# Optimization experiments

Measured on AMD Instinct MI355X. Metric: run time of the kernel, lower is better.

## Reference

```python
import jax, jax.numpy as jnp
import numpy as np

T = 16384      # total packed tokens
C = 1024       # d_model
H = 16         # n_head
HD = C // H    # head dim = 64
N_SEG = 32     # number of equal varlen segments
SEG = T // N_SEG


def setup_inputs() -> dict:
    key = jax.random.key(0)
    k1, k2, k3 = jax.random.split(key, 3)
    x = jax.random.normal(k1, (T, C), dtype=jnp.float32)
    w_attn = jax.random.normal(k2, (C, 3 * C), dtype=jnp.float32) * (1.0 / np.sqrt(C))
    w_proj = jax.random.normal(k3, (C, C), dtype=jnp.float32) * (1.0 / np.sqrt(C))
    # boundary indices for torch.tensor_split -> 32 equal segments of SEG tokens
    split_sections = (jnp.arange(1, N_SEG) * SEG).astype(jnp.int64)
    return {"x": x, "w_attn": w_attn, "w_proj": w_proj, "split_sections": split_sections}


def reference(x, w_attn, w_proj, split_sections):
    # x: [T, C] packed tokens; split_sections: 31 boundaries -> 32 equal segments
    n_seg = int(np.asarray(split_sections).shape[0]) + 1
    seg = x.shape[0] // n_seg
    qkv = x @ w_attn                                   # [T, 3C]
    q, k, v = jnp.split(qkv, 3, axis=-1)               # each [T, C]

    def heads(t):
        # [T, C] -> [H, n_seg, seg, HD]  (block-diagonal segment layout)
        return t.reshape(x.shape[0], H, HD).transpose(1, 0, 2).reshape(H, n_seg, seg, HD)

    q, k, v = heads(q), heads(k), heads(v)
    scale = 1.0 / np.sqrt(HD)
    att = jnp.einsum('hnqd,hnkd->hnqk', q, k) * scale  # [H, n_seg, seg, seg]
    att = jax.nn.softmax(att, axis=-1)
    y = jnp.einsum('hnqk,hnkd->hnqd', att, v)          # [H, n_seg, seg, HD]
    y = y.reshape(H, x.shape[0], HD).transpose(1, 0, 2).reshape(x.shape[0], C)
    return y @ w_proj                                  # [T, C]
```

## Files before the change

kernel.cpp:

```cpp
#include <hip/hip_runtime.h>
#include <hip/hip_bf16.h>
#include <stdint.h>

typedef __attribute__((ext_vector_type(8))) short short8;
typedef __attribute__((ext_vector_type(4))) short short4_t;
typedef __attribute__((ext_vector_type(4))) float float4_t;

#define GLOAD_LDS16(gp, lp)                                                              \
  __builtin_amdgcn_global_load_lds((const __attribute__((address_space(1))) unsigned int*)(gp), \
                                   (__attribute__((address_space(3))) unsigned int*)(lp), \
                                   16, 0, 0)

__device__ __forceinline__ float4_t mfma_bf16(short8 a, short8 b, float4_t c) {
  return __builtin_amdgcn_mfma_f32_16x16x32_bf16(a, b, c, 0, 0, 0);
}

__device__ __forceinline__ short f2bf(float f) {
  union { float f; unsigned int u; } v; v.f = f;
  unsigned int r = v.u + 0x7fff + ((v.u >> 16) & 1);
  return (short)(r >> 16);
}

__device__ __forceinline__ float red_sum16(float v) {
  v += __shfl_xor(v, 1);
  v += __shfl_xor(v, 2);
  v += __shfl_xor(v, 4);
  v += __shfl_xor(v, 8);
  return v;
}

__device__ __forceinline__ long swz_col(long colbase64, int chunk, int sub, int row) {
  return colbase64 + ((chunk ^ (row & 7)) << 3) + sub;
}

__global__ __launch_bounds__(256) void conv_swz(const float* __restrict__ in,
                                                short* __restrict__ out, long nchunks) {
  for (long ch = (long)blockIdx.x * blockDim.x + threadIdx.x; ch < nchunks;
       ch += (long)gridDim.x * blockDim.x) {
    long r  = ch >> 7;
    int cir = (int)(ch & 127);
    int pc  = (cir & ~3) | ((cir & 3) ^ (((int)r >> 1) & 3));
    const float* src = in + ch * 8;
    short8 o;
#pragma unroll
    for (int j = 0; j < 8; ++j) o[j] = f2bf(src[j]);
    *(short8*)&out[r * 1024 + pc * 8] = o;
  }
}

__global__ __launch_bounds__(256) void transpose_conv(const float* __restrict__ in,
                                                      short* __restrict__ out,
                                                      int R, int C) {
  __shared__ short tile[32][33];
  int c0 = blockIdx.x * 32;
  int r0 = blockIdx.y * 32;
  int tx = threadIdx.x;
  int ty = threadIdx.y;
#pragma unroll
  for (int i = 0; i < 4; ++i)
    tile[ty + i * 8][tx] = f2bf(in[(long)(r0 + ty + i * 8) * C + c0 + tx]);
  __syncthreads();
#pragma unroll
  for (int i = 0; i < 4; ++i) {
    int n   = c0 + ty + i * 8;
    long cc = (long)r0 + ((((tx >> 3) ^ ((n >> 1) & 3))) << 3) + (tx & 7);
    out[(long)n * R + cc] = tile[tx][ty + i * 8];
  }
}

template <int MODE>
__global__ __launch_bounds__(512, 2) void gemm256(const short* __restrict__ A, long lda,
                                                  const short* __restrict__ Bt, long ldb,
                                                  void* __restrict__ Cv,
                                                  short* __restrict__ vT,
                                                  int M, int N, int K) {
  __shared__ __align__(16) short As[4][256 * 32];
  __shared__ __align__(16) short Bs[4][256 * 32];

  const int tid  = threadIdx.x;
  const int wave = tid >> 6;
  const int lane = tid & 63;
  const int rA   = lane & 15;
  const int q4   = lane >> 4;
  const int wm   = (wave >> 2) * 128;
  const int wn   = (wave & 3) * 64;

  const int nbx = N >> 8;
  const int nwg = nbx * (M >> 8);
  const int bid = (int)blockIdx.y * nbx + (int)blockIdx.x;
  const int cpx = nwg >> 3;
  const int swz = (bid & 7) * cpx + (bid >> 3);
  const long m0 = (long)(swz / nbx) * 256;
  const long n0 = (long)(swz % nbx) * 256;

  const short* Ag = A  + (m0 + (tid >> 2)) * lda + (tid & 3) * 8;
  const short* Bg = Bt + (n0 + (tid >> 2)) * ldb + (tid & 3) * 8;

#define STAGE_A(u)                                                          \
  {                                                                         \
    const int slot_ = (u) & 3;                                              \
    GLOAD_LDS16(Ag + (u) * 32,             &As[slot_][wave * 512]);         \
    GLOAD_LDS16(Ag + 128 * lda + (u) * 32, &As[slot_][4096 + wave * 512]);  \
  }
#define STAGE_B(u)                                                          \
  {                                                                         \
    const int slot_ = (u) & 3;                                              \
    GLOAD_LDS16(Bg + (u) * 32,             &Bs[slot_][wave * 512]);         \
    GLOAD_LDS16(Bg + 128 * ldb + (u) * 32, &Bs[slot_][4096 + wave * 512]);  \
  }

  float4_t acc[8][4];
#pragma unroll
  for (int i = 0; i < 8; ++i)
#pragma unroll
    for (int j = 0; j < 4; ++j) acc[i][j] = (float4_t){0.f, 0.f, 0.f, 0.f};

  const int nt = K >> 5;

  STAGE_A(0); STAGE_B(0);
  STAGE_A(1); STAGE_B(1);
  STAGE_A(2); STAGE_B(2);
  asm volatile("s_waitcnt vmcnt(8)" ::: "memory");
  __builtin_amdgcn_s_barrier();

  const int cswz = q4 ^ ((rA >> 1) & 3);

  for (int u = 0; u < nt; ++u) {
    const int slot = u & 3;
    short8 af[4], bfr[4];
#pragma unroll
    for (int mi = 0; mi < 4; ++mi)
      af[mi] = *(const short8*)&As[slot][((wm + mi * 16 + rA) * 4 + cswz) * 8];
#pragma unroll
    for (int ni = 0; ni < 4; ++ni)
      bfr[ni] = *(const short8*)&Bs[slot][((wn + ni * 16 + rA) * 4 + cswz) * 8];
    if (u + 3 < nt) STAGE_A(u + 3);
    __builtin_amdgcn_s_barrier();
    __builtin_amdgcn_s_setprio(1);
#pragma unroll
    for (int mi = 0; mi < 4; ++mi)
#pragma unroll
      for (int ni = 0; ni < 4; ++ni)
        acc[mi][ni] = mfma_bf16(af[mi], bfr[ni], acc[mi][ni]);
    __builtin_amdgcn_s_setprio(0);
    __builtin_amdgcn_s_barrier();
#pragma unroll
    for (int mi = 0; mi < 4; ++mi)
      af[mi] = *(const short8*)&As[slot][((wm + 64 + mi * 16 + rA) * 4 + cswz) * 8];
    if (u + 3 < nt) STAGE_B(u + 3);
    __builtin_amdgcn_s_barrier();
    __builtin_amdgcn_s_setprio(1);
#pragma unroll
    for (int mi = 0; mi < 4; ++mi)
#pragma unroll
      for (int ni = 0; ni < 4; ++ni)
        acc[mi + 4][ni] = mfma_bf16(af[mi], bfr[ni], acc[mi + 4][ni]);
    __builtin_amdgcn_s_setprio(0);
    {
      const int rem = nt - 2 - u;
      if (rem >= 2)      asm volatile("s_waitcnt vmcnt(8)" ::: "memory");
      else if (rem == 1) asm volatile("s_waitcnt vmcnt(4)" ::: "memory");
      else               asm volatile("s_waitcnt vmcnt(0)" ::: "memory");
    }
    __builtin_amdgcn_s_barrier();
  }
#undef STAGE_A
#undef STAGE_B

  if constexpr (MODE == 1) {
    short* Cq = (short*)Cv;
    if (n0 >= 2048) {
#pragma unroll
      for (int mi = 0; mi < 8; ++mi) {
        int tbase = (int)m0 + wm + mi * 16 + q4 * 4;
        int ct    = (tbase >> 3) & 7;
#pragma unroll
        for (int ni = 0; ni < 4; ++ni) {
          int c = (int)n0 + wn + ni * 16 + rA;
          int d = c - 2048;
          long dst = (long)d * 16384 + (tbase & ~63) +
                     (((ct ^ (d & 7))) << 3) + (tbase & 7);
          short4_t o;
#pragma unroll
          for (int reg = 0; reg < 4; ++reg) o[reg] = f2bf(acc[mi][ni][reg]);
          *(short4_t*)&vT[dst] = o;
        }
      }
    } else {
#pragma unroll
      for (int mi = 0; mi < 8; ++mi)
#pragma unroll
        for (int ni = 0; ni < 4; ++ni)
#pragma unroll
          for (int reg = 0; reg < 4; ++reg) {
            long t = m0 + wm + mi * 16 + q4 * 4 + reg;
            int  c = (int)n0 + wn + ni * 16 + rA;
            long cc = swz_col((long)(c & ~63), (c >> 3) & 7, c & 7, (int)t);
            Cq[t * 3072 + cc] = f2bf(acc[mi][ni][reg]);
          }
    }
  } else {
    float* Co = (float*)Cv;
    (void)vT;
#pragma unroll
    for (int mi = 0; mi < 8; ++mi)
#pragma unroll
      for (int ni = 0; ni < 4; ++ni)
#pragma unroll
        for (int reg = 0; reg < 4; ++reg) {
          long row = m0 + wm + mi * 16 + q4 * 4 + reg;
          long col = n0 + wn + ni * 16 + rA;
          Co[row * (long)N + col] = acc[mi][ni][reg];
        }
  }
}

__global__ __launch_bounds__(256, 2) void attn_kernel(short* __restrict__ qkv,
                                                      const short* __restrict__ vT) {
  __shared__ __align__(16) short Qs[128 * 64];
  __shared__ __align__(16) short Ks[2][64 * 64];
  __shared__ __align__(16) short Vt[2][64 * 64];
  __shared__ __align__(16) short Ps[128 * 72];

  const int tid  = threadIdx.x;
  const int wave = tid >> 6;
  const int lane = tid & 63;
  const int rA   = lane & 15;
  const int q4   = lane >> 4;
  const int qt   = blockIdx.x;
  const int seg  = blockIdx.y;
  const int h    = blockIdx.z;

  const long tq0  = (long)seg * 512 + qt * 128;
  const long tk0  = (long)seg * 512;
  const long hoff = (long)h * 64;

#pragma unroll
  for (int i = 0; i < 4; ++i) {
    int slot = i * 256 + tid;
    int r    = slot >> 3;
    int c    = slot & 7;
    GLOAD_LDS16(qkv + (tq0 + r) * 3072 + hoff + c * 8, &Qs[(i * 256 + wave * 64) * 8]);
  }
#pragma unroll
  for (int i = 0; i < 2; ++i) {
    int slot = i * 256 + tid;
    int r    = slot >> 3;
    int c    = slot & 7;
    GLOAD_LDS16(qkv + (tk0 + r) * 3072 + 1024 + hoff + c * 8,
                &Ks[0][(i * 256 + wave * 64) * 8]);
    GLOAD_LDS16(vT + (hoff + r) * 16384 + tk0 + c * 8,
                &Vt[0][(i * 256 + wave * 64) * 8]);
  }

  float4_t acc_o[2][4];
  float l_st[2][4];
#pragma unroll
  for (int mi = 0; mi < 2; ++mi)
#pragma unroll
    for (int di = 0; di < 4; ++di) acc_o[mi][di] = (float4_t){0.f, 0.f, 0.f, 0.f};
#pragma unroll
  for (int mi = 0; mi < 2; ++mi)
#pragma unroll
    for (int reg = 0; reg < 4; ++reg) l_st[mi][reg] = 0.f;

  for (int kt = 0; kt < 8; ++kt) {
    const int p = kt & 1;
    __syncthreads();

    if (kt < 7) {
      const long tkn = tk0 + (kt + 1) * 64;
#pragma unroll
      for (int i = 0; i < 2; ++i) {
        int slot = i * 256 + tid;
        int r    = slot >> 3;
        int c    = slot & 7;
        GLOAD_LDS16(qkv + (tkn + r) * 3072 + 1024 + hoff + c * 8,
                    &Ks[1 - p][(i * 256 + wave * 64) * 8]);
        GLOAD_LDS16(vT + (hoff + r) * 16384 + tkn + c * 8,
                    &Vt[1 - p][(i * 256 + wave * 64) * 8]);
      }
    }

    float4_t s_acc[2][4];
#pragma unroll
    for (int mi = 0; mi < 2; ++mi)
#pragma unroll
      for (int ni = 0; ni < 4; ++ni) s_acc[mi][ni] = (float4_t){0.f, 0.f, 0.f, 0.f};
#pragma unroll
    for (int kk = 0; kk < 2; ++kk) {
      int cp = (kk * 4 + q4) ^ (rA & 7);
      short8 af[2], bfr[4];
#pragma unroll
      for (int mi = 0; mi < 2; ++mi) {
        int r  = wave * 32 + mi * 16 + rA;
        af[mi] = *(const short8*)&Qs[(r * 8 + cp) * 8];
      }
#pragma unroll
      for (int ni = 0; ni < 4; ++ni) {
        int r  = ni * 16 + rA;
        bfr[ni] = *(const short8*)&Ks[p][(r * 8 + cp) * 8];
      }
#pragma unroll
      for (int mi = 0; mi < 2; ++mi)
#pragma unroll
        for (int ni = 0; ni < 4; ++ni)
          s_acc[mi][ni] = mfma_bf16(af[mi], bfr[ni], s_acc[mi][ni]);
    }

#pragma unroll
    for (int mi = 0; mi < 2; ++mi)
#pragma unroll
      for (int reg = 0; reg < 4; ++reg) {
        float rs = 0.f;
#pragma unroll
        for (int ni = 0; ni < 4; ++ni) {
          float pv = __expf(s_acc[mi][ni][reg] * 0.125f);
          s_acc[mi][ni][reg] = pv;
          rs += pv;
        }
        l_st[mi][reg] += rs;
      }

#pragma unroll
    for (int mi = 0; mi < 2; ++mi)
#pragma unroll
      for (int ni = 0; ni < 4; ++ni)
#pragma unroll
        for (int reg = 0; reg < 4; ++reg)
          Ps[(wave * 32 + mi * 16 + q4 * 4 + reg) * 72 + ni * 16 + rA] =
              f2bf(s_acc[mi][ni][reg]);

    __syncthreads();

#pragma unroll
    for (int kk = 0; kk < 2; ++kk) {
      int cp = (kk * 4 + q4) ^ (rA & 7);
      short8 af[2], bfr[4];
#pragma unroll
      for (int mi = 0; mi < 2; ++mi)
        af[mi] = *(const short8*)&Ps[(wave * 32 + mi * 16 + rA) * 72 + (kk * 4 + q4) * 8];
#pragma unroll
      for (int di = 0; di < 4; ++di)
        bfr[di] = *(const short8*)&Vt[p][((di * 16 + rA) * 8 + cp) * 8];
#pragma unroll
      for (int mi = 0; mi < 2; ++mi)
#pragma unroll
        for (int di = 0; di < 4; ++di)
          acc_o[mi][di] = mfma_bf16(af[mi], bfr[di], acc_o[mi][di]);
    }
  }

#pragma unroll
  for (int mi = 0; mi < 2; ++mi)
#pragma unroll
    for (int reg = 0; reg < 4; ++reg) {
      float l  = red_sum16(l_st[mi][reg]);
      float rl = 1.0f / l;
      long t = tq0 + wave * 32 + mi * 16 + q4 * 4 + reg;
#pragma unroll
      for (int di = 0; di < 4; ++di) {
        int c  = di * 16 + rA;
        long cc = hoff + (c & 32) +
                  (((((c >> 3) & 3) ^ (((int)t >> 1) & 3))) << 3) + (c & 7);
        qkv[t * 3072 + cc] = f2bf(acc_o[mi][di][reg] * rl);
      }
    }
}

extern "C" void kernel_launch(void* const* d_in, const int* in_sizes, int n_in,
                              void* d_out, int out_size, void* d_ws, size_t ws_size,
                              hipStream_t stream) {
  const float* x      = (const float*)d_in[0];
  const float* w_attn = (const float*)d_in[1];
  const float* w_proj = (const float*)d_in[2];
  float* out = (float*)d_out;

  short* wT_a = (short*)d_ws;
  short* wT_p = wT_a + (size_t)3072 * 1024;
  short* qkv  = wT_p + (size_t)1024 * 1024;

  short* xb = (short*)d_out;
  short* vT = xb + (size_t)16384 * 1024;

  conv_swz<<<2048, 256, 0, stream>>>(x, xb, (long)16384 * 1024 / 8);
  transpose_conv<<<dim3(3072 / 32, 1024 / 32), dim3(32, 8), 0, stream>>>(w_attn, wT_a, 1024, 3072);
  transpose_conv<<<dim3(1024 / 32, 1024 / 32), dim3(32, 8), 0, stream>>>(w_proj, wT_p, 1024, 1024);

  gemm256<1><<<dim3(3072 / 256, 16384 / 256), 512, 0, stream>>>(xb, 1024, wT_a, 1024, qkv, vT,
                                                                16384, 3072, 1024);

  attn_kernel<<<dim3(4, 32, 16), 256, 0, stream>>>(qkv, vT);

  gemm256<2><<<dim3(1024 / 256, 16384 / 256), 512, 0, stream>>>(qkv, 3072, wT_p, 1024, out, nullptr,
                                                                16384, 1024, 1024);
}
```

Before: 366.1 us.

## Software-pipeline LDS fragment loads across K-tiles in GEMM main loop

```diff
diff --git a/kernel.cpp b/kernel.cpp
--- a/kernel.cpp
+++ b/kernel.cpp
@@ -116,6 +116,7 @@
     for (int j = 0; j < 4; ++j) acc[i][j] = (float4_t){0.f, 0.f, 0.f, 0.f};
 
   const int nt = K >> 5;
+  const int cswz = q4 ^ ((rA >> 1) & 3);
 
   STAGE_A(0); STAGE_B(0);
   STAGE_A(1); STAGE_B(1);
@@ -123,46 +124,57 @@
   asm volatile("s_waitcnt vmcnt(8)" ::: "memory");
   __builtin_amdgcn_s_barrier();
 
-  const int cswz = q4 ^ ((rA >> 1) & 3);
-
-  for (int u = 0; u < nt; ++u) {
+  short8 afl[4], afh[4], bf0[4], bf1[4];
+#pragma unroll
+  for (int mi = 0; mi < 4; ++mi)
+    afl[mi] = *(const short8*)&As[0][((wm + mi * 16 + rA) * 4 + cswz) * 8];
+#pragma unroll
+  for (int ni = 0; ni < 4; ++ni)
+    bf0[ni] = *(const short8*)&Bs[0][((wn + ni * 16 + rA) * 4 + cswz) * 8];
+
+  auto tile_step = [&](int u, short8 (&bc)[4], short8 (&bn)[4]) {
     const int slot = u & 3;
-    short8 af[4], bfr[4];
 #pragma unroll
     for (int mi = 0; mi < 4; ++mi)
-      af[mi] = *(const short8*)&As[slot][((wm + mi * 16 + rA) * 4 + cswz) * 8];
-#pragma unroll
-    for (int ni = 0; ni < 4; ++ni)
-      bfr[ni] = *(const short8*)&Bs[slot][((wn + ni * 16 + rA) * 4 + cswz) * 8];
+      afh[mi] = *(const short8*)&As[slot][((wm + 64 + mi * 16 + rA) * 4 + cswz) * 8];
     if (u + 3 < nt) STAGE_A(u + 3);
+    asm volatile("s_waitcnt lgkmcnt(4)" ::: "memory");
+    __builtin_amdgcn_s_setprio(1);
+#pragma unroll
+    for (int mi = 0; mi < 4; ++mi)
+#pragma unroll
+      for (int ni = 0; ni < 4; ++ni)
+        acc[mi][ni] = mfma_bf16(afl[mi], bc[ni], acc[mi][ni]);
+    __builtin_amdgcn_s_setprio(0);
+    if (u + 3 < nt)      asm volatile("s_waitcnt vmcnt(6)" ::: "memory");
+    else if (u + 2 < nt) asm volatile("s_waitcnt vmcnt(4)" ::: "memory");
+    else                 asm volatile("s_waitcnt vmcnt(0)" ::: "memory");
     __builtin_amdgcn_s_barrier();
+    if (u + 1 < nt) {
+      const int ns = (u + 1) & 3;
+#pragma unroll
+      for (int mi = 0; mi < 4; ++mi)
+        afl[mi] = *(const short8*)&As[ns][((wm + mi * 16 + rA) * 4 + cswz) * 8];
+#pragma unroll
+      for (int ni = 0; ni < 4; ++ni)
+        bn[ni] = *(const short8*)&Bs[ns][((wn + ni * 16 + rA) * 4 + cswz) * 8];
+    }
+    if (u + 3 < nt) STAGE_B(u + 3);
+    if (u + 1 < nt) asm volatile("s_waitcnt lgkmcnt(8)" ::: "memory");
+    else            asm volatile("s_waitcnt lgkmcnt(0)" ::: "memory");
     __builtin_amdgcn_s_setprio(1);
 #pragma unroll
     for (int mi = 0; mi < 4; ++mi)
 #pragma unroll
       for (int ni = 0; ni < 4; ++ni)
-        acc[mi][ni] = mfma_bf16(af[mi], bfr[ni], acc[mi][ni]);
+        acc[mi + 4][ni] = mfma_bf16(afh[mi], bc[ni], acc[mi + 4][ni]);
     __builtin_amdgcn_s_setprio(0);
     __builtin_amdgcn_s_barrier();
-#pragma unroll
-    for (int mi = 0; mi < 4; ++mi)
-      af[mi] = *(const short8*)&As[slot][((wm + 64 + mi * 16 + rA) * 4 + cswz) * 8];
-    if (u + 3 < nt) STAGE_B(u + 3);
-    __builtin_amdgcn_s_barrier();
-    __builtin_amdgcn_s_setprio(1);
-#pragma unroll
-    for (int mi = 0; mi < 4; ++mi)
-#pragma unroll
-      for (int ni = 0; ni < 4; ++ni)
-        acc[mi + 4][ni] = mfma_bf16(af[mi], bfr[ni], acc[mi + 4][ni]);
-    __builtin_amdgcn_s_setprio(0);
-    {
-      const int rem = nt - 2 - u;
-      if (rem >= 2)      asm volatile("s_waitcnt vmcnt(8)" ::: "memory");
-      else if (rem == 1) asm volatile("s_waitcnt vmcnt(4)" ::: "memory");
-      else               asm volatile("s_waitcnt vmcnt(0)" ::: "memory");
-    }
-    __builtin_amdgcn_s_barrier();
+  };
+
+  for (int u = 0; u < nt; u += 2) {
+    tile_step(u,     bf0, bf1);
+    tile_step(u + 1, bf1, bf0);
   }
 #undef STAGE_A
 #undef STAGE_B
```

Result: faster. 353.0 us (-3.6%).
